# Optimization experiments

Measured on AMD Instinct MI355X. Metric: run time of the kernel, lower is better.

## Reference

```python
import jax, jax.numpy as jnp
import numpy as np

HIDDEN = 4096
NQ = 32        # query heads
NKV = 8        # kv heads
HD = 128       # head dim
EPS = 1e-6
BASE = 10000.0
T = 2048


def setup_inputs() -> dict:
    key = jax.random.key(0)
    ks = jax.random.split(key, 4)
    s = 0.02
    return {
        "hidden_states": jax.random.normal(ks[0], (T, HIDDEN), jnp.float32),
        "w_qkv": jax.random.normal(ks[1], ((NQ + 2 * NKV) * HD, HIDDEN), jnp.float32) * s,
        "q_norm_w": jnp.ones((HD,), jnp.float32),
        "k_norm_w": jnp.ones((HD,), jnp.float32),
        "w_o": jax.random.normal(ks[2], (HIDDEN, NQ * HD), jnp.float32) * s,
        "positions": jnp.arange(T, dtype=jnp.int64),
    }


def _rms_norm(x, w):
    # x: [T, H, D], normalize over last dim
    var = jnp.mean(jnp.square(x), axis=-1, keepdims=True)
    return x * jax.lax.rsqrt(var + EPS) * w


def _rope(x, positions):
    # neox-style: split halves. x: [T, H, D]
    half = HD // 2
    inv_freq = 1.0 / (BASE ** (jnp.arange(0, HD, 2, dtype=jnp.float32) / HD))  # [half]
    ang = positions.astype(jnp.float32)[:, None] * inv_freq  # [T, half]
    cos = jnp.cos(ang)[:, None, :]  # [T, 1, half]
    sin = jnp.sin(ang)[:, None, :]
    x1, x2 = x[..., :half], x[..., half:]
    return jnp.concatenate([x1 * cos - x2 * sin, x2 * cos + x1 * sin], axis=-1)


def reference(hidden_states, w_qkv, q_norm_w, k_norm_w, w_o, positions):
    t = hidden_states.shape[0]
    qkv = hidden_states @ w_qkv.T  # [T, (NQ+2*NKV)*HD]
    q, k, v = jnp.split(qkv, [NQ * HD, (NQ + NKV) * HD], axis=-1)
    q = _rms_norm(q.reshape(t, NQ, HD), q_norm_w)
    k = _rms_norm(k.reshape(t, NKV, HD), k_norm_w)
    v = v.reshape(t, NKV, HD)
    q = _rope(q, positions)
    k = _rope(k, positions)

    g = NQ // NKV
    qg = q.reshape(t, NKV, g, HD).transpose(1, 2, 0, 3)  # [NKV, g, T, HD]
    kt = k.transpose(1, 0, 2)  # [NKV, T, HD]
    vt = v.transpose(1, 0, 2)
    scale = HD ** -0.5
    scores = jnp.einsum('hgqd,hkd->hgqk', qg, kt) * scale  # [NKV, g, T, T]
    causal = positions[:, None] >= positions[None, :]  # [T, T]
    scores = jnp.where(causal[None, None], scores, jnp.float32(-1e30))
    p = jax.nn.softmax(scores, axis=-1)
    o = jnp.einsum('hgqk,hkd->hgqd', p, vt)  # [NKV, g, T, HD]
    o = o.transpose(2, 0, 1, 3).reshape(t, NQ * HD)
    return o @ w_o.T
```

## Files before the change

### kernel.cpp

```cpp
#include <hip/hip_runtime.h>
#include <hip/hip_bf16.h>

typedef float f32x4 __attribute__((ext_vector_type(4)));
typedef short s16x8 __attribute__((ext_vector_type(8)));
typedef short s16x4 __attribute__((ext_vector_type(4)));
typedef unsigned short u16;

#define HIDDEN 4096
#define NQ 32
#define NKV 8
#define HD 128
#define T_SEQ 2048
#define QKV_N ((NQ + 2 * NKV) * HD)

__device__ __forceinline__ u16 f2bf(float f) {
    union { float f; unsigned u; } v; v.f = f;
    unsigned r = v.u + 0x7FFFu + ((v.u >> 16) & 1u);
    return (u16)(r >> 16);
}
__device__ __forceinline__ float b2f(u16 h) {
    union { unsigned u; float f; } v; v.u = ((unsigned)h) << 16; return v.f;
}
__device__ __forceinline__ void gload_lds16(const u16* g, u16* l) {
    __builtin_amdgcn_global_load_lds(
        (const __attribute__((address_space(1))) unsigned int*)g,
        (__attribute__((address_space(3))) unsigned int*)l,
        16, 0, 0);
}

__global__ __launch_bounds__(256) void conv_bf16_kern(
    const float* __restrict__ src, u16* __restrict__ dst, int n8)
{
    for (int i = blockIdx.x * 256 + threadIdx.x; i < n8; i += gridDim.x * 256) {
        const float4 a = ((const float4*)src)[2 * i];
        const float4 b = ((const float4*)src)[2 * i + 1];
        s16x8 o;
        o[0] = (short)f2bf(a.x); o[1] = (short)f2bf(a.y);
        o[2] = (short)f2bf(a.z); o[3] = (short)f2bf(a.w);
        o[4] = (short)f2bf(b.x); o[5] = (short)f2bf(b.y);
        o[6] = (short)f2bf(b.z); o[7] = (short)f2bf(b.w);
        ((s16x8*)dst)[i] = o;
    }
}

template<int OUT_BF16>
__global__ __launch_bounds__(256) void gemm_bt_bf16(
    const u16* __restrict__ A, const u16* __restrict__ B,
    void* __restrict__ Cv, int N, int K)
{
    __shared__ u16 As[2][128 * 32];
    __shared__ u16 Bs[2][128 * 32];
    const int tid = threadIdx.x, lane = tid & 63, wid = tid >> 6;
    const int wr = wid >> 1, wc = wid & 1, lg = lane >> 4, l15 = lane & 15;
    const int m0 = blockIdx.y * 128, n0 = blockIdx.x * 128;
    const int srow = wid * 32 + (lane >> 2);
    const int scol = (lane & 3) * 8;
    const u16* ga = &A[(size_t)(m0 + srow) * K + scol];
    const u16* gb = &B[(size_t)(n0 + srow) * K + scol];

    f32x4 acc[4][4] = {};
    const int nk = K >> 5;

    auto stage = [&](int buf, int koff) {
        u16* la = &As[buf][wid * 1024];
        u16* lb = &Bs[buf][wid * 1024];
        gload_lds16(ga + koff, la);
        gload_lds16(ga + koff + 16 * K, la + 512);
        gload_lds16(gb + koff, lb);
        gload_lds16(gb + koff + 16 * K, lb + 512);
    };

    stage(0, 0);
    __syncthreads();
    for (int kk = 0; kk < nk; ++kk) {
        const int cur = kk & 1;
        if (kk + 1 < nk) stage(cur ^ 1, (kk + 1) * 32);
        s16x8 af[4], bfr[4];
#pragma unroll
        for (int i = 0; i < 4; ++i) af[i]  = *(const s16x8*)&As[cur][(wr * 64 + i * 16 + l15) * 32 + lg * 8];
#pragma unroll
        for (int j = 0; j < 4; ++j) bfr[j] = *(const s16x8*)&Bs[cur][(wc * 64 + j * 16 + l15) * 32 + lg * 8];
#pragma unroll
        for (int i = 0; i < 4; ++i)
#pragma unroll
            for (int j = 0; j < 4; ++j)
                acc[i][j] = __builtin_amdgcn_mfma_f32_16x16x32_bf16(af[i], bfr[j], acc[i][j], 0, 0, 0);
        __syncthreads();
    }
#pragma unroll
    for (int i = 0; i < 4; ++i) {
        int r0 = m0 + wr * 64 + i * 16 + lg * 4;
#pragma unroll
        for (int j = 0; j < 4; ++j) {
            int cc = n0 + wc * 64 + j * 16 + l15;
#pragma unroll
            for (int r = 0; r < 4; ++r) {
                if (OUT_BF16)
                    ((u16*)Cv)[(size_t)(r0 + r) * N + cc] = f2bf(acc[i][j][r]);
                else
                    ((float*)Cv)[(size_t)(r0 + r) * N + cc] = acc[i][j][r];
            }
        }
    }
}

__global__ __launch_bounds__(64) void norm_rope_kern(
    const u16* __restrict__ qkv, const float* __restrict__ qw,
    const float* __restrict__ kw, u16* __restrict__ qr, u16* __restrict__ kr)
{
    const int t = blockIdx.x, h = blockIdx.y, i = threadIdx.x;
    const size_t rowbase = (size_t)t * QKV_N;
    const u16* src; const float* w; u16* dst;
    if (h < 32) {
        src = qkv + rowbase + h * HD; w = qw;
        dst = qr + ((size_t)h * T_SEQ + t) * HD;
    } else {
        int kh = h - 32;
        src = qkv + rowbase + NQ * HD + kh * HD; w = kw;
        dst = kr + ((size_t)kh * T_SEQ + t) * HD;
    }
    float x1 = b2f(src[i]), x2 = b2f(src[i + 64]);
    float ss = x1 * x1 + x2 * x2;
#pragma unroll
    for (int d = 32; d >= 1; d >>= 1) ss += __shfl_xor(ss, d);
    float rs = rsqrtf(ss * (1.0f / 128.0f) + 1e-6f);
    x1 *= rs * w[i];
    x2 *= rs * w[i + 64];
    float ang = (float)t * powf(10000.0f, -(float)i * (1.0f / 64.0f));
    float sn, cs;
    sincosf(ang, &sn, &cs);
    dst[i]      = f2bf(x1 * cs - x2 * sn);
    dst[i + 64] = f2bf(x2 * cs + x1 * sn);
}

__global__ __launch_bounds__(256) void vtrans_kern(
    const u16* __restrict__ qkv, u16* __restrict__ vt)
{
    __shared__ u16 Ts[128][66];
    const int t0 = blockIdx.x * 64, kh = blockIdx.y, tid = threadIdx.x;
#pragma unroll
    for (int it = 0; it < 4; ++it) {
        int slot = tid + it * 256;
        int tl = slot >> 4, dc = (slot & 15) * 8;
        s16x8 v = *(const s16x8*)&qkv[(size_t)(t0 + tl) * QKV_N + (NQ + NKV) * HD + kh * HD + dc];
#pragma unroll
        for (int e = 0; e < 8; ++e) Ts[dc + e][tl] = (u16)v[e];
    }
    __syncthreads();
#pragma unroll
    for (int it = 0; it < 4; ++it) {
        int slot = tid + it * 256;
        int d = slot >> 3, c = (slot & 7) * 8;
        s16x8 v = *(const s16x8*)&Ts[d][c];
        *(s16x8*)&vt[((size_t)kh * HD + d) * T_SEQ + t0 + c] = v;
    }
}

#define KS(r, c) Ks[((r) << 7) + ((c) ^ (((r) & 7) << 3))]
#define VS(r, c) Vs[((r) << 6) + ((c) ^ (((r) & 7) << 3))]
#define PS(wv, r, c) Ps[((wv) << 10) + ((r) << 6) + ((c) ^ (((r) & 7) << 3))]

__global__ __launch_bounds__(512) void attn_kern(
    const u16* __restrict__ qr, const u16* __restrict__ kr,
    const u16* __restrict__ vt, u16* __restrict__ o)
{
    __shared__ u16 Ks[64 * 128];
    __shared__ u16 Vs[128 * 64];
    __shared__ u16 Ps[8 * 16 * 64];
    const int tid = threadIdx.x, lane = tid & 63, w = tid >> 6;
    const int lg = lane >> 4, l15 = lane & 15;
    const int qh = blockIdx.y, kvh = qh >> 2;
    const float scale2 = 0.08838834764831845f * 1.4426950408889634f;

    const int krow = tid >> 4, kcol = (tid & 15) * 8;
    const int vrow = tid >> 3, vcol = (tid & 7) * 8;
    const u16* krbase = kr + (size_t)kvh * T_SEQ * HD;
    const u16* vtbase = vt + (size_t)kvh * HD * T_SEQ;

    s16x8 kst[2], vst[2];
#define LOADKV(k0_) do { \
    kst[0] = *(const s16x8*)&krbase[(size_t)((k0_) + krow) * HD + kcol]; \
    kst[1] = *(const s16x8*)&krbase[(size_t)((k0_) + krow + 32) * HD + kcol]; \
    vst[0] = *(const s16x8*)&vtbase[(size_t)(vrow) * T_SEQ + (k0_) + vcol]; \
    vst[1] = *(const s16x8*)&vtbase[(size_t)(vrow + 64) * T_SEQ + (k0_) + vcol]; \
    } while (0)

    for (int half = 0; half < 2; ++half) {
        const int q0 = (half == 0) ? (int)blockIdx.x * 128
                                   : (T_SEQ - 128) - (int)blockIdx.x * 128;
        s16x8 qf[4];
        {
            const u16* qb = qr + ((size_t)qh * T_SEQ + q0 + w * 16 + l15) * HD;
#pragma unroll
            for (int dc = 0; dc < 4; ++dc) qf[dc] = *(const s16x8*)&qb[dc * 32 + lg * 8];
        }
        f32x4 oacc[8] = {};
        float mQ = -1e30f, lsQ = 0.f;

        const int ktiles = (q0 >> 6) + 2;
        LOADKV(0);
        for (int kt = 0; kt < ktiles; ++kt) {
            const int k0 = kt * 64;
            __syncthreads();
            *(s16x8*)&KS(krow, kcol) = kst[0];
            *(s16x8*)&KS(krow + 32, kcol) = kst[1];
            *(s16x8*)&VS(vrow, vcol) = vst[0];
            *(s16x8*)&VS(vrow + 64, vcol) = vst[1];
            __syncthreads();
            if (kt + 1 < ktiles) LOADKV(k0 + 64);

            f32x4 sc[4] = {};
            __builtin_amdgcn_s_setprio(1);
#pragma unroll
            for (int nc = 0; nc < 4; ++nc)
#pragma unroll
                for (int dc = 0; dc < 4; ++dc) {
                    s16x8 kf = *(const s16x8*)&KS(nc * 16 + l15, dc * 32 + lg * 8);
                    sc[nc] = __builtin_amdgcn_mfma_f32_16x16x32_bf16(kf, qf[dc], sc[nc], 0, 0, 0);
                }
            __builtin_amdgcn_s_setprio(0);

            const int qg = q0 + w * 16 + l15;
            const bool needMask = (k0 + 63) > (q0 + w * 16);
            float tm = -1e30f;
#pragma unroll
            for (int nc = 0; nc < 4; ++nc)
#pragma unroll
                for (int r = 0; r < 4; ++r) {
                    float v = sc[nc][r] * scale2;
                    int kg = k0 + nc * 16 + lg * 4 + r;
                    if (needMask && kg > qg) v = -1e30f;
                    sc[nc][r] = v;
                    tm = fmaxf(tm, v);
                }
            tm = fmaxf(tm, __shfl_xor(tm, 16));
            tm = fmaxf(tm, __shfl_xor(tm, 32));

            if (__any(tm > mQ + 8.0f)) {
                float mn = fmaxf(mQ, tm);
                float alpha = exp2f(mQ - mn);
                mQ = mn;
                lsQ *= alpha;
                float aq[4];
#pragma unroll
                for (int r = 0; r < 4; ++r) aq[r] = __shfl(alpha, lg * 4 + r);
#pragma unroll
                for (int dc = 0; dc < 8; ++dc)
#pragma unroll
                    for (int r = 0; r < 4; ++r) oacc[dc][r] *= aq[r];
            }

            float ts = 0.f;
#pragma unroll
            for (int nc = 0; nc < 4; ++nc) {
                s16x4 pk;
#pragma unroll
                for (int r = 0; r < 4; ++r) {
                    float e = exp2f(sc[nc][r] - mQ);
                    ts += e;
                    pk[r] = (short)f2bf(e);
                }
                *(s16x4*)&PS(w, l15, nc * 16 + lg * 4) = pk;
            }
            ts += __shfl_xor(ts, 16);
            ts += __shfl_xor(ts, 32);
            lsQ += ts;

            __builtin_amdgcn_s_setprio(1);
#pragma unroll
            for (int kc = 0; kc < 2; ++kc) {
                s16x8 pf = *(const s16x8*)&PS(w, l15, kc * 32 + lg * 8);
#pragma unroll
                for (int dc = 0; dc < 8; ++dc) {
                    s16x8 vf = *(const s16x8*)&VS(dc * 16 + l15, kc * 32 + lg * 8);
                    oacc[dc] = __builtin_amdgcn_mfma_f32_16x16x32_bf16(pf, vf, oacc[dc], 0, 0, 0);
                }
            }
            __builtin_amdgcn_s_setprio(0);
        }
        float lq[4];
#pragma unroll
        for (int r = 0; r < 4; ++r) lq[r] = __shfl(lsQ, lg * 4 + r);
#pragma unroll
        for (int r = 0; r < 4; ++r) {
            float inv = 1.0f / lq[r];
            int trow = q0 + w * 16 + lg * 4 + r;
            u16* dst = o + (size_t)trow * (NQ * HD) + qh * HD;
#pragma unroll
            for (int dc = 0; dc < 8; ++dc) dst[dc * 16 + l15] = f2bf(oacc[dc][r] * inv);
        }
    }
#undef LOADKV
}

extern "C" void kernel_launch(void* const* d_in, const int* in_sizes, int n_in,
                              void* d_out, int out_size, void* d_ws, size_t ws_size,
                              hipStream_t stream)
{
    const float* hs   = (const float*)d_in[0];
    const float* wqkv = (const float*)d_in[1];
    const float* qw   = (const float*)d_in[2];
    const float* kw   = (const float*)d_in[3];
    const float* wo   = (const float*)d_in[4];
    float* out = (float*)d_out;

    char* ws = (char*)d_ws;
    u16* hs_bf   = (u16*)(ws);
    u16* ob      = (u16*)(ws);
    u16* wqkv_bf = (u16*)(ws + 16777216);
    u16* qr      = (u16*)(ws + 16777216);
    u16* kr      = (u16*)(ws + 33554432);
    u16* vt      = (u16*)(ws + 37748736);
    u16* wo_bf   = (u16*)(ws + 41943040);
    u16* qkv_bf  = (u16*)(ws + 67108864);

    conv_bf16_kern<<<2048, 256, 0, stream>>>(hs, hs_bf, T_SEQ * HIDDEN / 8);
    conv_bf16_kern<<<2048, 256, 0, stream>>>(wqkv, wqkv_bf, QKV_N * HIDDEN / 8);
    gemm_bt_bf16<1><<<dim3(QKV_N / 128, T_SEQ / 128), 256, 0, stream>>>(
        hs_bf, wqkv_bf, (void*)qkv_bf, QKV_N, HIDDEN);
    norm_rope_kern<<<dim3(T_SEQ, 40), 64, 0, stream>>>(qkv_bf, qw, kw, qr, kr);
    vtrans_kern<<<dim3(T_SEQ / 64, NKV), 256, 0, stream>>>(qkv_bf, vt);
    conv_bf16_kern<<<2048, 256, 0, stream>>>(wo, wo_bf, HIDDEN * HIDDEN / 8);
    attn_kern<<<dim3(8, NQ), 512, 0, stream>>>(qr, kr, vt, ob);
    gemm_bt_bf16<0><<<dim3(HIDDEN / 128, T_SEQ / 128), 256, 0, stream>>>(
        ob, wo_bf, (void*)out, HIDDEN, HIDDEN);
}
```

Measured before the change: 364.0 us.

## Swizzle GEMM LDS, remap workgroups across XCDs, fix waitcnt, widen norm-rope blocks

```diff
diff --git a/kernel.cpp b/kernel.cpp
--- a/kernel.cpp
+++ b/kernel.cpp
@@ -26,6 +26,9 @@
         (const __attribute__((address_space(1))) unsigned int*)g,
         (__attribute__((address_space(3))) unsigned int*)l,
         16, 0, 0);
+}
+__device__ __forceinline__ int xcd_swz(int flat, int nwg) {
+    return (flat & 7) * (nwg >> 3) + (flat >> 3);
 }
 
 __global__ __launch_bounds__(256) void conv_bf16_kern(
@@ -52,11 +55,14 @@
     __shared__ u16 Bs[2][128 * 32];
     const int tid = threadIdx.x, lane = tid & 63, wid = tid >> 6;
     const int wr = wid >> 1, wc = wid & 1, lg = lane >> 4, l15 = lane & 15;
-    const int m0 = blockIdx.y * 128, n0 = blockIdx.x * 128;
+    const int nwg = gridDim.x * gridDim.y;
+    const int flat = xcd_swz((int)blockIdx.y * gridDim.x + (int)blockIdx.x, nwg);
+    const int m0 = (flat / gridDim.x) * 128, n0 = (flat % gridDim.x) * 128;
     const int srow = wid * 32 + (lane >> 2);
-    const int scol = (lane & 3) * 8;
+    const int scol = (((lane & 3) ^ ((lane >> 3) & 3))) * 8;
     const u16* ga = &A[(size_t)(m0 + srow) * K + scol];
     const u16* gb = &B[(size_t)(n0 + srow) * K + scol];
+    const int rsw = (lg ^ ((l15 >> 1) & 3)) * 8;
 
     f32x4 acc[4][4] = {};
     const int nk = K >> 5;
@@ -71,21 +77,26 @@
     };
 
     stage(0, 0);
-    __syncthreads();
     for (int kk = 0; kk < nk; ++kk) {
         const int cur = kk & 1;
-        if (kk + 1 < nk) stage(cur ^ 1, (kk + 1) * 32);
+        if (kk + 1 < nk) {
+            stage(cur ^ 1, (kk + 1) * 32);
+            asm volatile("s_waitcnt vmcnt(4)" ::: "memory");
+        } else {
+            asm volatile("s_waitcnt vmcnt(0)" ::: "memory");
+        }
+        __builtin_amdgcn_s_barrier();
         s16x8 af[4], bfr[4];
 #pragma unroll
-        for (int i = 0; i < 4; ++i) af[i]  = *(const s16x8*)&As[cur][(wr * 64 + i * 16 + l15) * 32 + lg * 8];
-#pragma unroll
-        for (int j = 0; j < 4; ++j) bfr[j] = *(const s16x8*)&Bs[cur][(wc * 64 + j * 16 + l15) * 32 + lg * 8];
+        for (int i = 0; i < 4; ++i) af[i]  = *(const s16x8*)&As[cur][(wr * 64 + i * 16 + l15) * 32 + rsw];
+#pragma unroll
+        for (int j = 0; j < 4; ++j) bfr[j] = *(const s16x8*)&Bs[cur][(wc * 64 + j * 16 + l15) * 32 + rsw];
 #pragma unroll
         for (int i = 0; i < 4; ++i)
 #pragma unroll
             for (int j = 0; j < 4; ++j)
                 acc[i][j] = __builtin_amdgcn_mfma_f32_16x16x32_bf16(af[i], bfr[j], acc[i][j], 0, 0, 0);
-        __syncthreads();
+        __builtin_amdgcn_s_barrier();
     }
 #pragma unroll
     for (int i = 0; i < 4; ++i) {
@@ -104,11 +115,12 @@
     }
 }
 
-__global__ __launch_bounds__(64) void norm_rope_kern(
+__global__ __launch_bounds__(256) void norm_rope_kern(
     const u16* __restrict__ qkv, const float* __restrict__ qw,
     const float* __restrict__ kw, u16* __restrict__ qr, u16* __restrict__ kr)
 {
-    const int t = blockIdx.x, h = blockIdx.y, i = threadIdx.x;
+    const int t = blockIdx.x, h = blockIdx.y * 4 + (threadIdx.x >> 6);
+    const int i = threadIdx.x & 63;
     const size_t rowbase = (size_t)t * QKV_N;
     const u16* src; const float* w; u16* dst;
     if (h < 32) {
@@ -169,7 +181,9 @@
     __shared__ u16 Ps[8 * 16 * 64];
     const int tid = threadIdx.x, lane = tid & 63, w = tid >> 6;
     const int lg = lane >> 4, l15 = lane & 15;
-    const int qh = blockIdx.y, kvh = qh >> 2;
+    const int flat = xcd_swz((int)blockIdx.y * 8 + (int)blockIdx.x, 256);
+    const int qh = flat >> 3, bx = flat & 7;
+    const int kvh = qh >> 2;
     const float scale2 = 0.08838834764831845f * 1.4426950408889634f;
 
     const int krow = tid >> 4, kcol = (tid & 15) * 8;
@@ -186,8 +200,7 @@
     } while (0)
 
     for (int half = 0; half < 2; ++half) {
-        const int q0 = (half == 0) ? (int)blockIdx.x * 128
-                                   : (T_SEQ - 128) - (int)blockIdx.x * 128;
+        const int q0 = (half == 0) ? bx * 128 : (T_SEQ - 128) - bx * 128;
         s16x8 qf[4];
         {
             const u16* qb = qr + ((size_t)qh * T_SEQ + q0 + w * 16 + l15) * HD;
@@ -318,7 +331,7 @@
     conv_bf16_kern<<<2048, 256, 0, stream>>>(wqkv, wqkv_bf, QKV_N * HIDDEN / 8);
     gemm_bt_bf16<1><<<dim3(QKV_N / 128, T_SEQ / 128), 256, 0, stream>>>(
         hs_bf, wqkv_bf, (void*)qkv_bf, QKV_N, HIDDEN);
-    norm_rope_kern<<<dim3(T_SEQ, 40), 64, 0, stream>>>(qkv_bf, qw, kw, qr, kr);
+    norm_rope_kern<<<dim3(T_SEQ, 10), 256, 0, stream>>>(qkv_bf, qw, kw, qr, kr);
     vtrans_kern<<<dim3(T_SEQ / 64, NKV), 256, 0, stream>>>(qkv_bf, vt);
     conv_bf16_kern<<<2048, 256, 0, stream>>>(wo, wo_bf, HIDDEN * HIDDEN / 8);
     attn_kern<<<dim3(8, NQ), 512, 0, stream>>>(qr, kr, vt, ob);
```

Measured after the change: 366.2 us. About the same (+0.6%).
